# Performance work log

Measured on AMD Instinct MI355X. Metric: run time of the kernel, lower is better.

## Reference

```python
import jax, jax.numpy as jnp
import numpy as np

N_HEAD, N_KV_HEAD, N_EMBD, SEQ_LEN = 16, 4, 1024, 2048
HEAD_DIM = N_EMBD // N_HEAD  # 64
B = 2


def _rope(x, cos, sin):
    # x: [B, T, H, D]; cos/sin: [1, T, 1, D//2]
    d = x.shape[-1] // 2
    x1, x2 = x[..., :d], x[..., d:]
    return jnp.concatenate([x1 * cos + x2 * sin, -x1 * sin + x2 * cos], axis=-1)


def setup_inputs() -> dict:
    key = jax.random.key(0)
    ks = jax.random.split(key, 5)
    x = jax.random.normal(ks[0], (B, SEQ_LEN, N_EMBD), dtype=jnp.float32)
    # real RoPE tables (base 10000)
    half = HEAD_DIM // 2
    inv_freq = 1.0 / (10000.0 ** (jnp.arange(half, dtype=jnp.float32) / half))
    ang = jnp.arange(SEQ_LEN, dtype=jnp.float32)[:, None] * inv_freq[None, :]  # [T, half]
    cos = jnp.cos(ang)[None, :, None, :]  # [1, T, 1, half]
    sin = jnp.sin(ang)[None, :, None, :]
    s = 0.02
    Wq = s * jax.random.normal(ks[1], (N_EMBD, N_HEAD * HEAD_DIM), dtype=jnp.float32)
    Wk = s * jax.random.normal(ks[2], (N_EMBD, N_KV_HEAD * HEAD_DIM), dtype=jnp.float32)
    Wv = s * jax.random.normal(ks[3], (N_EMBD, N_KV_HEAD * HEAD_DIM), dtype=jnp.float32)
    Wo = s * jax.random.normal(ks[4], (N_EMBD, N_EMBD), dtype=jnp.float32)
    return {"x": x, "cos": cos, "sin": sin, "Wq": Wq, "Wk": Wk, "Wv": Wv, "Wo": Wo}


def reference(x, cos, sin, Wq, Wk, Wv, Wo):
    Bsz, T, C = x.shape
    H, Hkv, D = N_HEAD, N_KV_HEAD, HEAD_DIM
    q = (x @ Wq).reshape(Bsz, T, H, D)
    k = (x @ Wk).reshape(Bsz, T, Hkv, D)
    v = (x @ Wv).reshape(Bsz, T, Hkv, D)
    q = _rope(q, cos, sin)
    k = _rope(k, cos, sin)
    # GQA: repeat kv heads to match query heads
    rep = H // Hkv
    k = jnp.repeat(k, rep, axis=2)  # [B, T, H, D]
    v = jnp.repeat(v, rep, axis=2)
    scale = 1.0 / np.sqrt(D).astype(np.float32)
    att = jnp.einsum('bqhd,bkhd->bhqk', q, k) * scale  # [B, H, T, T]
    causal = jnp.tril(jnp.ones((T, T), dtype=bool))
    att = jnp.where(causal[None, None, :, :], att, -jnp.inf)
    att = jax.nn.softmax(att, axis=-1)
    y = jnp.einsum('bhqk,bkhd->bqhd', att, v).reshape(Bsz, T, C)
    return y @ Wo
```

## Files before the change

kernel.cpp:

```cpp
#include <hip/hip_runtime.h>
#include <hip/hip_bf16.h>


typedef __attribute__((ext_vector_type(8))) short s16x8;
typedef __attribute__((ext_vector_type(4))) float f32x4;
typedef __attribute__((ext_vector_type(4))) unsigned short u16x4;

#define LOG2E 1.44269504088896340736f

__device__ __forceinline__ float bf2f(unsigned short u) {
  unsigned int i = ((unsigned int)u) << 16;
  return __builtin_bit_cast(float, i);
}
__device__ __forceinline__ unsigned short f2bf(float f) {
  unsigned int i = __builtin_bit_cast(unsigned int, f);
  i += 0x7fffu + ((i >> 16) & 1u);
  return (unsigned short)(i >> 16);
}

__device__ __forceinline__ void async16(const void* g, void* l) {
  __builtin_amdgcn_global_load_lds(
      (const __attribute__((address_space(1))) void*)g,
      (__attribute__((address_space(3))) void*)l, 16, 0, 0);
}


__global__ void conv_f32_to_bf16(const float* __restrict__ in,
                                 unsigned short* __restrict__ out, int n) {
  int i = (blockIdx.x * blockDim.x + threadIdx.x) * 4;
  if (i + 3 < n) {
    float4 v = *(const float4*)(in + i);
    u16x4 o = { f2bf(v.x), f2bf(v.y), f2bf(v.z), f2bf(v.w) };
    *(u16x4*)(out + i) = o;
  }
}

__global__ void transpose_conv(const float* __restrict__ W,
                               unsigned short* __restrict__ Wt, int K, int N) {
  __shared__ float tile[32][33];
  int n0 = blockIdx.x * 32, k0 = blockIdx.y * 32;
  int tx = threadIdx.x, ty = threadIdx.y;
  for (int i = ty; i < 32; i += 8)
    tile[i][tx] = W[(size_t)(k0 + i) * N + n0 + tx];
  __syncthreads();
  for (int i = ty; i < 32; i += 8)
    Wt[(size_t)(n0 + i) * K + k0 + tx] = f2bf(tile[tx][i]);
}

__global__ void rope_qk(unsigned short* __restrict__ QKV,
                        const float* __restrict__ cosb,
                        const float* __restrict__ sinb) {
  int idx = blockIdx.x * blockDim.x + threadIdx.x;
  int d = idx & 31;
  int hh = (idx >> 5) % 20;
  int row = idx / (32 * 20);
  int t = row & 2047;
  size_t base;
  float mul;
  if (hh < 16) { base = (size_t)row * 1536 + hh * 64 + d;               mul = 0.125f; }
  else         { base = (size_t)row * 1536 + 1024 + (hh - 16) * 64 + d; mul = 1.0f;   }
  float x1 = bf2f(QKV[base]), x2 = bf2f(QKV[base + 32]);
  float c = cosb[t * 32 + d], s = sinb[t * 32 + d];
  QKV[base]      = f2bf((x1 * c + x2 * s) * mul);
  QKV[base + 32] = f2bf((-x1 * s + x2 * c) * mul);
}

__global__ __launch_bounds__(256) void gemm_bt(
    const unsigned short* __restrict__ A, const unsigned short* __restrict__ Bt,
    void* __restrict__ Cp, int M, int N, int K, int c_f32) {
  __shared__ unsigned short As[128 * 64];
  __shared__ unsigned short Bs[64 * 64];
  int tid = threadIdx.x;
  int w = tid >> 6, l = tid & 63, g = l >> 4, lr = l & 15;
  int wr = w >> 1, wc = w & 1;
  int m0 = blockIdx.y * 128, n0 = blockIdx.x * 64;
  int sk = lr & 7;

  f32x4 acc[4][2] = {};

  for (int k0 = 0; k0 < K; k0 += 64) {
#pragma unroll
    for (int i = 0; i < 4; ++i) {
      int c = i * 256 + tid;
      int row = c >> 3, srcu = ((c & 7) ^ (row & 7)) * 8;
      async16(A + (size_t)(m0 + row) * K + k0 + srcu, (char*)As + c * 16);
    }
#pragma unroll
    for (int i = 0; i < 2; ++i) {
      int c = i * 256 + tid;
      int row = c >> 3, srcu = ((c & 7) ^ (row & 7)) * 8;
      async16(Bt + (size_t)(n0 + row) * K + k0 + srcu, (char*)Bs + c * 16);
    }
    __syncthreads();

    s16x8 af[2][4], bfr[2][2];
#pragma unroll
    for (int ks = 0; ks < 2; ++ks) {
#pragma unroll
      for (int m = 0; m < 4; ++m)
        af[ks][m] = *(const s16x8*)(As + (wr * 64 + m * 16 + lr) * 64 +
                                    ((ks * 4 + g) ^ sk) * 8);
#pragma unroll
      for (int n = 0; n < 2; ++n)
        bfr[ks][n] = *(const s16x8*)(Bs + (wc * 32 + n * 16 + lr) * 64 +
                                     ((ks * 4 + g) ^ sk) * 8);
    }
#pragma unroll
    for (int ks = 0; ks < 2; ++ks)
#pragma unroll
      for (int m = 0; m < 4; ++m)
#pragma unroll
        for (int n = 0; n < 2; ++n)
          acc[m][n] = __builtin_amdgcn_mfma_f32_16x16x32_bf16(
              af[ks][m], bfr[ks][n], acc[m][n], 0, 0, 0);
    __syncthreads();
  }

  if (c_f32) {
    float* C = (float*)Cp;
#pragma unroll
    for (int m = 0; m < 4; ++m)
#pragma unroll
      for (int n = 0; n < 2; ++n)
#pragma unroll
        for (int r = 0; r < 4; ++r)
          C[(size_t)(m0 + wr * 64 + m * 16 + g * 4 + r) * N +
            n0 + wc * 32 + n * 16 + lr] = acc[m][n][r];
  } else {
    unsigned short* C = (unsigned short*)Cp;
#pragma unroll
    for (int m = 0; m < 4; ++m)
#pragma unroll
      for (int n = 0; n < 2; ++n)
#pragma unroll
        for (int r = 0; r < 4; ++r)
          C[(size_t)(m0 + wr * 64 + m * 16 + g * 4 + r) * N +
            n0 + wc * 32 + n * 16 + lr] = f2bf(acc[m][n][r]);
  }
}

__global__ __launch_bounds__(256) void attn_fused(
    const unsigned short* __restrict__ QKV, unsigned short* __restrict__ Y) {
  __shared__ unsigned short Kt[2][64 * 64];
  __shared__ unsigned short Vt[2][64 * 64];
  __shared__ unsigned short Pb[4][16 * 64];

  const int T = 2048, CS = 1536;
  int tid = threadIdx.x;
  int w = tid >> 6, l = tid & 63, g = l >> 4, lr = l & 15;
  int n = blockIdx.x;
  int ip = n >> 5;
  int bh = n & 31, b = bh >> 4, h = bh & 15, kvh = h >> 2;
  int sx = lr & 7;

  const unsigned short* Qp = QKV + (size_t)b * T * CS + h * 64;
  const unsigned short* Kp = QKV + (size_t)b * T * CS + 1024 + kvh * 64;
  const unsigned short* Vp = QKV + (size_t)b * T * CS + 1280 + kvh * 64;
  unsigned short* Pw = Pb[w];

  int kvA = tid & 63, dA = (tid >> 6) * 8, dB = dA + 32;

  for (int pass = 0; pass < 2; ++pass) {
    int qt = pass == 0 ? (31 - ip) : ip;
    int qw = qt * 64 + w * 16;
    int q_mine = qw + lr;

    s16x8 qf[2];
#pragma unroll
    for (int ks = 0; ks < 2; ++ks)
      qf[ks] = *(const s16x8*)(Qp + (size_t)q_mine * CS + ks * 32 + g * 8);

    f32x4 o[4] = {};
    float mrun = -1e30f, lrun = 0.f;
    int ntiles = qt + 1;

#pragma unroll
    for (int i = 0; i < 2; ++i) {
      int c = i * 256 + tid;
      int row = c >> 3, srcc = ((c & 7) ^ (row & 7)) * 8;
      async16(Kp + (size_t)row * CS + srcc, (char*)(&Kt[0][0]) + c * 16);
    }
#pragma unroll
    for (int i = 0; i < 2; ++i) {
      int c = i * 256 + tid;
      int kv = c & 63, d0v = (c >> 6) * 8;
      s16x8 vv = *(const s16x8*)(Vp + (size_t)kv * CS + d0v);
#pragma unroll
      for (int j = 0; j < 8; ++j)
        Vt[0][(d0v + j) * 64 + (kv ^ (j * 8))] = (unsigned short)vv[j];
    }
    __syncthreads();

    int cur = 0;
    for (int it = 0; it < ntiles; ++it) {
      int kv0 = it * 64;
      bool hasnext = (it + 1 < ntiles);

      s16x8 vvA, vvB;
      if (hasnext) {
        int kvn = kv0 + 64;
#pragma unroll
        for (int i = 0; i < 2; ++i) {
          int c = i * 256 + tid;
          int row = c >> 3, srcc = ((c & 7) ^ (row & 7)) * 8;
          async16(Kp + (size_t)(kvn + row) * CS + srcc,
                  (char*)(&Kt[cur ^ 1][0]) + c * 16);
        }
        vvA = *(const s16x8*)(Vp + (size_t)(kvn + kvA) * CS + dA);
        vvB = *(const s16x8*)(Vp + (size_t)(kvn + kvA) * CS + dB);
      }

      const unsigned short* Kc = &Kt[cur][0];
      const unsigned short* Vc = &Vt[cur][0];
      f32x4 s[4];
      __builtin_amdgcn_s_setprio(1);
#pragma unroll
      for (int nf = 0; nf < 4; ++nf) {
        f32x4 z = {};
#pragma unroll
        for (int ks = 0; ks < 2; ++ks) {
          s16x8 kf = *(const s16x8*)(Kc + (nf * 16 + lr) * 64 +
                                     ((ks * 4 + g) ^ sx) * 8);
          z = __builtin_amdgcn_mfma_f32_16x16x32_bf16(kf, qf[ks], z, 0, 0, 0);
        }
        s[nf] = z;
      }
      __builtin_amdgcn_s_setprio(0);

      if (it == ntiles - 1) {
#pragma unroll
        for (int nf = 0; nf < 4; ++nf)
#pragma unroll
          for (int r = 0; r < 4; ++r)
            if (kv0 + nf * 16 + g * 4 + r > q_mine) s[nf][r] = -1e30f;
      }

      float mt = s[0][0];
#pragma unroll
      for (int nf = 0; nf < 4; ++nf)
#pragma unroll
        for (int r = 0; r < 4; ++r) mt = fmaxf(mt, s[nf][r]);
      mt = fmaxf(mt, __shfl_xor(mt, 16, 64));
      mt = fmaxf(mt, __shfl_xor(mt, 32, 64));

      if (__any(mt > mrun + 8.f)) {
        float mnew = fmaxf(mrun, mt);
        float corr = exp2f((mrun - mnew) * LOG2E);
        float psum = 0.f;
#pragma unroll
        for (int nf = 0; nf < 4; ++nf)
#pragma unroll
          for (int r = 0; r < 4; ++r) {
            float p = exp2f((s[nf][r] - mnew) * LOG2E);
            s[nf][r] = p;
            psum += p;
          }
        psum += __shfl_xor(psum, 16, 64);
        psum += __shfl_xor(psum, 32, 64);
        lrun = lrun * corr + psum;
        mrun = mnew;
#pragma unroll
        for (int r = 0; r < 4; ++r) {
          float cr = __shfl(corr, g * 4 + r, 64);
#pragma unroll
          for (int d0 = 0; d0 < 4; ++d0) o[d0][r] *= cr;
        }
      } else {
        float psum = 0.f;
#pragma unroll
        for (int nf = 0; nf < 4; ++nf)
#pragma unroll
          for (int r = 0; r < 4; ++r) {
            float p = exp2f((s[nf][r] - mrun) * LOG2E);
            s[nf][r] = p;
            psum += p;
          }
        psum += __shfl_xor(psum, 16, 64);
        psum += __shfl_xor(psum, 32, 64);
        lrun += psum;
      }

#pragma unroll
      for (int nf = 0; nf < 4; ++nf) {
        u16x4 pv = { f2bf(s[nf][0]), f2bf(s[nf][1]),
                     f2bf(s[nf][2]), f2bf(s[nf][3]) };
        *(u16x4*)(Pw + lr * 64 + ((nf * 16 + g * 4) ^ (sx * 8))) = pv;
      }
      asm volatile("s_waitcnt lgkmcnt(0)" ::: "memory");
      __builtin_amdgcn_sched_barrier(0);

      s16x8 pf[2];
#pragma unroll
      for (int ks = 0; ks < 2; ++ks)
        pf[ks] = *(const s16x8*)(Pw + lr * 64 + ((ks * 4 + g) ^ sx) * 8);
      __builtin_amdgcn_s_setprio(1);
#pragma unroll
      for (int d0 = 0; d0 < 4; ++d0)
#pragma unroll
        for (int ks = 0; ks < 2; ++ks) {
          s16x8 vf = *(const s16x8*)(Vc + (d0 * 16 + lr) * 64 +
                                     ((ks * 4 + g) ^ sx) * 8);
          o[d0] = __builtin_amdgcn_mfma_f32_16x16x32_bf16(pf[ks], vf, o[d0], 0, 0, 0);
        }
      __builtin_amdgcn_s_setprio(0);

      if (hasnext) {
#pragma unroll
        for (int j = 0; j < 8; ++j)
          Vt[cur ^ 1][(dA + j) * 64 + (kvA ^ (j * 8))] = (unsigned short)vvA[j];
#pragma unroll
        for (int j = 0; j < 8; ++j)
          Vt[cur ^ 1][(dB + j) * 64 + (kvA ^ (j * 8))] = (unsigned short)vvB[j];
      }
      __syncthreads();
      cur ^= 1;
    }

#pragma unroll
    for (int r = 0; r < 4; ++r) {
      float lv = __shfl(lrun, g * 4 + r, 64);
      float inv = 1.f / lv;
      size_t rowoff = (size_t)(b * T + qw + g * 4 + r) * 1024 + h * 64;
#pragma unroll
      for (int d0 = 0; d0 < 4; ++d0)
        Y[rowoff + d0 * 16 + lr] = f2bf(o[d0][r] * inv);
    }
  }
}


extern "C" void kernel_launch(void* const* d_in, const int* in_sizes, int n_in,
                              void* d_out, int out_size, void* d_ws, size_t ws_size,
                              hipStream_t stream) {
  const float* x    = (const float*)d_in[0];
  const float* cosb = (const float*)d_in[1];
  const float* sinb = (const float*)d_in[2];
  const float* Wq   = (const float*)d_in[3];
  const float* Wk   = (const float*)d_in[4];
  const float* Wv   = (const float*)d_in[5];
  const float* Wo   = (const float*)d_in[6];
  float* out = (float*)d_out;

  char* ob = (char*)d_out;
  char* ws = (char*)d_ws;
  const size_t MB = 1024 * 1024;
  unsigned short* QKVb  = (unsigned short*)(ob);
  unsigned short* xb    = (unsigned short*)(ws);
  unsigned short* Wqkvt = (unsigned short*)(ws + 8 * MB);
  unsigned short* Wot   = (unsigned short*)(ws + 11 * MB);
  unsigned short* Yb    = xb;

  conv_f32_to_bf16<<<4096, 256, 0, stream>>>(x, xb, 4096 * 1024);
  transpose_conv<<<dim3(32, 32), dim3(32, 8), 0, stream>>>(Wq, Wqkvt, 1024, 1024);
  transpose_conv<<<dim3(8, 32), dim3(32, 8), 0, stream>>>(Wk, Wqkvt + (size_t)1024 * 1024, 1024, 256);
  transpose_conv<<<dim3(8, 32), dim3(32, 8), 0, stream>>>(Wv, Wqkvt + (size_t)1280 * 1024, 1024, 256);
  transpose_conv<<<dim3(32, 32), dim3(32, 8), 0, stream>>>(Wo, Wot, 1024, 1024);

  gemm_bt<<<dim3(24, 32), 256, 0, stream>>>(xb, Wqkvt, QKVb, 4096, 1536, 1024, 0);

  rope_qk<<<10240, 256, 0, stream>>>(QKVb, cosb, sinb);

  attn_fused<<<dim3(512), 256, 0, stream>>>(QKVb, Yb);

  gemm_bt<<<dim3(16, 32), 256, 0, stream>>>(Yb, Wot, out, 4096, 1024, 1024, 1);
}
```

Baseline: 132.7 us.

## Split attention KV range across two wave groups and merge partial softmax states

Attention blocks now run 512 threads as two groups of four waves, each handling half of the causal KV tiles for the same query tile, with per-group double-buffered K/V in shared memory. The partial output, max and sum from group 1 are merged into group 0 through shared memory at the end. This shortens the serial KV loop per block so more waves are in flight. It also folds log2(e) into the Q scaling during RoPE to drop a multiply per exp, and uses a packed bf16 convert instruction for P. In exchange it adds an end-of-pass merge, extra barriers, and idle waves when the two halves are uneven.

```diff
diff --git a/kernel.cpp b/kernel.cpp
--- a/kernel.cpp
+++ b/kernel.cpp
@@ -16,6 +16,11 @@
   unsigned int i = __builtin_bit_cast(unsigned int, f);
   i += 0x7fffu + ((i >> 16) & 1u);
   return (unsigned short)(i >> 16);
+}
+__device__ __forceinline__ unsigned int cvtpk(float lo, float hi) {
+  unsigned int r;
+  asm("v_cvt_pk_bf16_f32 %0, %1, %2" : "=v"(r) : "v"(lo), "v"(hi));
+  return r;
 }
 
 __device__ __forceinline__ void async16(const void* g, void* l) {
@@ -57,8 +62,8 @@
   int t = row & 2047;
   size_t base;
   float mul;
-  if (hh < 16) { base = (size_t)row * 1536 + hh * 64 + d;               mul = 0.125f; }
-  else         { base = (size_t)row * 1536 + 1024 + (hh - 16) * 64 + d; mul = 1.0f;   }
+  if (hh < 16) { base = (size_t)row * 1536 + hh * 64 + d;   mul = 0.125f * LOG2E; }
+  else         { base = (size_t)row * 1536 + 1024 + (hh - 16) * 64 + d; mul = 1.0f; }
   float x1 = bf2f(QKV[base]), x2 = bf2f(QKV[base + 32]);
   float c = cosb[t * 32 + d], s = sinb[t * 32 + d];
   QKV[base]      = f2bf((x1 * c + x2 * s) * mul);
@@ -139,30 +144,39 @@
   }
 }
 
-__global__ __launch_bounds__(256) void attn_fused(
+__global__ __launch_bounds__(512, 4) void attn_fused(
     const unsigned short* __restrict__ QKV, unsigned short* __restrict__ Y) {
-  __shared__ unsigned short Kt[2][64 * 64];
-  __shared__ unsigned short Vt[2][64 * 64];
-  __shared__ unsigned short Pb[4][16 * 64];
+  __shared__ char smem[81920];
 
   const int T = 2048, CS = 1536;
   int tid = threadIdx.x;
   int w = tid >> 6, l = tid & 63, g = l >> 4, lr = l & 15;
+  int grp = w >> 2, ws = w & 3, gt = tid & 255;
   int n = blockIdx.x;
   int ip = n >> 5;
   int bh = n & 31, b = bh >> 4, h = bh & 15, kvh = h >> 2;
   int sx = lr & 7;
 
+  unsigned short* Kg = (unsigned short*)(smem + grp * 16384);
+  unsigned short* Vg = (unsigned short*)(smem + 32768 + grp * 16384);
+  unsigned short* Pw = (unsigned short*)(smem + 65536 + w * 2048);
+  float* MO = (float*)(smem);
+  float* MM = (float*)(smem + 16384);
+  float* ML = (float*)(smem + 17408);
+
   const unsigned short* Qp = QKV + (size_t)b * T * CS + h * 64;
   const unsigned short* Kp = QKV + (size_t)b * T * CS + 1024 + kvh * 64;
   const unsigned short* Vp = QKV + (size_t)b * T * CS + 1280 + kvh * 64;
-  unsigned short* Pw = Pb[w];
-
-  int kvA = tid & 63, dA = (tid >> 6) * 8, dB = dA + 32;
+
+  int kvA = gt & 63, dA = (gt >> 6) * 8, dB = dA + 32;
 
   for (int pass = 0; pass < 2; ++pass) {
-    int qt = pass == 0 ? (31 - ip) : ip;
-    int qw = qt * 64 + w * 16;
+    int qt = pass ? ip : (31 - ip);
+    int nt = qt + 1;
+    int H1 = (nt + 1) >> 1;
+    int t0 = grp ? H1 : 0;
+    int cnt = grp ? (nt - H1) : H1;
+    int qw = qt * 64 + ws * 16;
     int q_mine = qw + lr;
 
     s16x8 qf[2];
@@ -172,158 +186,189 @@
 
     f32x4 o[4] = {};
     float mrun = -1e30f, lrun = 0.f;
-    int ntiles = qt + 1;
-
-#pragma unroll
-    for (int i = 0; i < 2; ++i) {
-      int c = i * 256 + tid;
-      int row = c >> 3, srcc = ((c & 7) ^ (row & 7)) * 8;
-      async16(Kp + (size_t)row * CS + srcc, (char*)(&Kt[0][0]) + c * 16);
-    }
-#pragma unroll
-    for (int i = 0; i < 2; ++i) {
-      int c = i * 256 + tid;
-      int kv = c & 63, d0v = (c >> 6) * 8;
-      s16x8 vv = *(const s16x8*)(Vp + (size_t)kv * CS + d0v);
-#pragma unroll
-      for (int j = 0; j < 8; ++j)
-        Vt[0][(d0v + j) * 64 + (kv ^ (j * 8))] = (unsigned short)vv[j];
-    }
+
     __syncthreads();
 
+    if (cnt > 0) {
+#pragma unroll
+      for (int i = 0; i < 2; ++i) {
+        int c = i * 256 + gt;
+        int row = c >> 3, srcc = ((c & 7) ^ (row & 7)) * 8;
+        async16(Kp + (size_t)(t0 * 64 + row) * CS + srcc, (char*)Kg + c * 16);
+      }
+#pragma unroll
+      for (int i = 0; i < 2; ++i) {
+        int c = i * 256 + gt;
+        int kv = c & 63, d0v = (c >> 6) * 8;
+        s16x8 vv = *(const s16x8*)(Vp + (size_t)(t0 * 64 + kv) * CS + d0v);
+#pragma unroll
+        for (int j = 0; j < 8; ++j)
+          Vg[(d0v + j) * 64 + (kv ^ (j * 8))] = (unsigned short)vv[j];
+      }
+    }
+    __syncthreads();
+
     int cur = 0;
-    for (int it = 0; it < ntiles; ++it) {
-      int kv0 = it * 64;
-      bool hasnext = (it + 1 < ntiles);
+    for (int j = 0; j < H1; ++j) {
+      int tj = t0 + j;
+      bool active = (j < cnt);
+      bool hasnext = (j + 1 < cnt);
+      int kv0 = tj * 64;
 
       s16x8 vvA, vvB;
       if (hasnext) {
         int kvn = kv0 + 64;
 #pragma unroll
         for (int i = 0; i < 2; ++i) {
-          int c = i * 256 + tid;
+          int c = i * 256 + gt;
           int row = c >> 3, srcc = ((c & 7) ^ (row & 7)) * 8;
           async16(Kp + (size_t)(kvn + row) * CS + srcc,
-                  (char*)(&Kt[cur ^ 1][0]) + c * 16);
+                  (char*)Kg + (cur ^ 1) * 8192 + c * 16);
         }
         vvA = *(const s16x8*)(Vp + (size_t)(kvn + kvA) * CS + dA);
         vvB = *(const s16x8*)(Vp + (size_t)(kvn + kvA) * CS + dB);
       }
 
-      const unsigned short* Kc = &Kt[cur][0];
-      const unsigned short* Vc = &Vt[cur][0];
-      f32x4 s[4];
-      __builtin_amdgcn_s_setprio(1);
-#pragma unroll
-      for (int nf = 0; nf < 4; ++nf) {
-        f32x4 z = {};
-#pragma unroll
-        for (int ks = 0; ks < 2; ++ks) {
-          s16x8 kf = *(const s16x8*)(Kc + (nf * 16 + lr) * 64 +
-                                     ((ks * 4 + g) ^ sx) * 8);
-          z = __builtin_amdgcn_mfma_f32_16x16x32_bf16(kf, qf[ks], z, 0, 0, 0);
-        }
-        s[nf] = z;
-      }
-      __builtin_amdgcn_s_setprio(0);
-
-      if (it == ntiles - 1) {
+      if (active) {
+        const unsigned short* Kc = Kg + cur * 4096;
+        const unsigned short* Vc = Vg + cur * 4096;
+        f32x4 s[4];
+        __builtin_amdgcn_s_setprio(1);
+#pragma unroll
+        for (int nf = 0; nf < 4; ++nf) {
+          f32x4 z = {};
+#pragma unroll
+          for (int ks = 0; ks < 2; ++ks) {
+            s16x8 kf = *(const s16x8*)(Kc + (nf * 16 + lr) * 64 +
+                                       ((ks * 4 + g) ^ sx) * 8);
+            z = __builtin_amdgcn_mfma_f32_16x16x32_bf16(kf, qf[ks], z, 0, 0, 0);
+          }
+          s[nf] = z;
+        }
+        __builtin_amdgcn_s_setprio(0);
+
+        if (tj == nt - 1) {
+#pragma unroll
+          for (int nf = 0; nf < 4; ++nf)
+#pragma unroll
+            for (int r = 0; r < 4; ++r)
+              if (kv0 + nf * 16 + g * 4 + r > q_mine) s[nf][r] = -1e30f;
+        }
+
+        float mt = s[0][0];
 #pragma unroll
         for (int nf = 0; nf < 4; ++nf)
 #pragma unroll
-          for (int r = 0; r < 4; ++r)
-            if (kv0 + nf * 16 + g * 4 + r > q_mine) s[nf][r] = -1e30f;
-      }
-
-      float mt = s[0][0];
-#pragma unroll
-      for (int nf = 0; nf < 4; ++nf)
-#pragma unroll
-        for (int r = 0; r < 4; ++r) mt = fmaxf(mt, s[nf][r]);
-      mt = fmaxf(mt, __shfl_xor(mt, 16, 64));
-      mt = fmaxf(mt, __shfl_xor(mt, 32, 64));
-
-      if (__any(mt > mrun + 8.f)) {
-        float mnew = fmaxf(mrun, mt);
-        float corr = exp2f((mrun - mnew) * LOG2E);
-        float psum = 0.f;
-#pragma unroll
-        for (int nf = 0; nf < 4; ++nf)
+          for (int r = 0; r < 4; ++r) mt = fmaxf(mt, s[nf][r]);
+        mt = fmaxf(mt, __shfl_xor(mt, 16, 64));
+        mt = fmaxf(mt, __shfl_xor(mt, 32, 64));
+
+        if (__any(mt > mrun + 11.5416f)) {
+          float mnew = fmaxf(mrun, mt);
+          float corr = exp2f(mrun - mnew);
+          float psum = 0.f;
+#pragma unroll
+          for (int nf = 0; nf < 4; ++nf)
+#pragma unroll
+            for (int r = 0; r < 4; ++r) {
+              float p = exp2f(s[nf][r] - mnew);
+              s[nf][r] = p;
+              psum += p;
+            }
+          psum += __shfl_xor(psum, 16, 64);
+          psum += __shfl_xor(psum, 32, 64);
+          lrun = lrun * corr + psum;
+          mrun = mnew;
 #pragma unroll
           for (int r = 0; r < 4; ++r) {
-            float p = exp2f((s[nf][r] - mnew) * LOG2E);
-            s[nf][r] = p;
-            psum += p;
+            float cr = __shfl(corr, g * 4 + r, 64);
+#pragma unroll
+            for (int d0 = 0; d0 < 4; ++d0) o[d0][r] *= cr;
           }
-        psum += __shfl_xor(psum, 16, 64);
-        psum += __shfl_xor(psum, 32, 64);
-        lrun = lrun * corr + psum;
-        mrun = mnew;
-#pragma unroll
-        for (int r = 0; r < 4; ++r) {
-          float cr = __shfl(corr, g * 4 + r, 64);
-#pragma unroll
-          for (int d0 = 0; d0 < 4; ++d0) o[d0][r] *= cr;
-        }
-      } else {
-        float psum = 0.f;
-#pragma unroll
-        for (int nf = 0; nf < 4; ++nf)
-#pragma unroll
-          for (int r = 0; r < 4; ++r) {
-            float p = exp2f((s[nf][r] - mrun) * LOG2E);
-            s[nf][r] = p;
-            psum += p;
+        } else {
+          float psum = 0.f;
+#pragma unroll
+          for (int nf = 0; nf < 4; ++nf)
+#pragma unroll
+            for (int r = 0; r < 4; ++r) {
+              float p = exp2f(s[nf][r] - mrun);
+              s[nf][r] = p;
+              psum += p;
+            }
+          psum += __shfl_xor(psum, 16, 64);
+          psum += __shfl_xor(psum, 32, 64);
+          lrun += psum;
+        }
+
+#pragma unroll
+        for (int nf = 0; nf < 4; ++nf) {
+          uint2 pv;
+          pv.x = cvtpk(s[nf][0], s[nf][1]);
+          pv.y = cvtpk(s[nf][2], s[nf][3]);
+          *(uint2*)(Pw + lr * 64 + ((nf * 16 + g * 4) ^ (sx * 8))) = pv;
+        }
+        asm volatile("s_waitcnt lgkmcnt(0)" ::: "memory");
+        __builtin_amdgcn_sched_barrier(0);
+
+        s16x8 pf[2];
+#pragma unroll
+        for (int ks = 0; ks < 2; ++ks)
+          pf[ks] = *(const s16x8*)(Pw + lr * 64 + ((ks * 4 + g) ^ sx) * 8);
+        __builtin_amdgcn_s_setprio(1);
+#pragma unroll
+        for (int d0 = 0; d0 < 4; ++d0)
+#pragma unroll
+          for (int ks = 0; ks < 2; ++ks) {
+            s16x8 vf = *(const s16x8*)(Vc + (d0 * 16 + lr) * 64 +
+                                       ((ks * 4 + g) ^ sx) * 8);
+            o[d0] = __builtin_amdgcn_mfma_f32_16x16x32_bf16(pf[ks], vf, o[d0], 0, 0, 0);
           }
-        psum += __shfl_xor(psum, 16, 64);
-        psum += __shfl_xor(psum, 32, 64);
-        lrun += psum;
-      }
-
-#pragma unroll
-      for (int nf = 0; nf < 4; ++nf) {
-        u16x4 pv = { f2bf(s[nf][0]), f2bf(s[nf][1]),
-                     f2bf(s[nf][2]), f2bf(s[nf][3]) };
-        *(u16x4*)(Pw + lr * 64 + ((nf * 16 + g * 4) ^ (sx * 8))) = pv;
-      }
-      asm volatile("s_waitcnt lgkmcnt(0)" ::: "memory");
-      __builtin_amdgcn_sched_barrier(0);
-
-      s16x8 pf[2];
-#pragma unroll
-      for (int ks = 0; ks < 2; ++ks)
-        pf[ks] = *(const s16x8*)(Pw + lr * 64 + ((ks * 4 + g) ^ sx) * 8);
-      __builtin_amdgcn_s_setprio(1);
-#pragma unroll
-      for (int d0 = 0; d0 < 4; ++d0)
-#pragma unroll
-        for (int ks = 0; ks < 2; ++ks) {
-          s16x8 vf = *(const s16x8*)(Vc + (d0 * 16 + lr) * 64 +
-                                     ((ks * 4 + g) ^ sx) * 8);
-          o[d0] = __builtin_amdgcn_mfma_f32_16x16x32_bf16(pf[ks], vf, o[d0], 0, 0, 0);
-        }
-      __builtin_amdgcn_s_setprio(0);
+        __builtin_amdgcn_s_setprio(0);
+      }
 
       if (hasnext) {
 #pragma unroll
-        for (int j = 0; j < 8; ++j)
-          Vt[cur ^ 1][(dA + j) * 64 + (kvA ^ (j * 8))] = (unsigned short)vvA[j];
-#pragma unroll
-        for (int j = 0; j < 8; ++j)
-          Vt[cur ^ 1][(dB + j) * 64 + (kvA ^ (j * 8))] = (unsigned short)vvB[j];
+        for (int j2 = 0; j2 < 8; ++j2)
+          Vg[cur == 0 ? 4096 + (dA + j2) * 64 + (kvA ^ (j2 * 8))
+                      : (dA + j2) * 64 + (kvA ^ (j2 * 8))] = (unsigned short)vvA[j2];
+#pragma unroll
+        for (int j2 = 0; j2 < 8; ++j2)
+          Vg[cur == 0 ? 4096 + (dB + j2) * 64 + (kvA ^ (j2 * 8))
+                      : (dB + j2) * 64 + (kvA ^ (j2 * 8))] = (unsigned short)vvB[j2];
       }
       __syncthreads();
       cur ^= 1;
     }
 
-#pragma unroll
-    for (int r = 0; r < 4; ++r) {
-      float lv = __shfl(lrun, g * 4 + r, 64);
-      float inv = 1.f / lv;
-      size_t rowoff = (size_t)(b * T + qw + g * 4 + r) * 1024 + h * 64;
+    int mbase = ws * 64 + l;
+    if (grp == 1) {
 #pragma unroll
       for (int d0 = 0; d0 < 4; ++d0)
-        Y[rowoff + d0 * 16 + lr] = f2bf(o[d0][r] * inv);
+#pragma unroll
+        for (int r = 0; r < 4; ++r)
+          MO[(d0 * 4 + r) * 256 + mbase] = o[d0][r];
+      MM[mbase] = mrun;
+      ML[mbase] = lrun;
+    }
+    __syncthreads();
+    if (grp == 0) {
+      float m1 = MM[mbase], l1 = ML[mbase];
+      float mS = fmaxf(mrun, m1);
+      float c0 = exp2f(mrun - mS), c1 = exp2f(m1 - mS);
+      float lS = lrun * c0 + l1 * c1;
+#pragma unroll
+      for (int r = 0; r < 4; ++r) {
+        float cr0 = __shfl(c0, g * 4 + r, 64);
+        float cr1 = __shfl(c1, g * 4 + r, 64);
+        float lv  = __shfl(lS, g * 4 + r, 64);
+        float inv = 1.f / lv;
+        size_t rowoff = (size_t)(b * T + qw + g * 4 + r) * 1024 + h * 64;
+#pragma unroll
+        for (int d0 = 0; d0 < 4; ++d0) {
+          float om = o[d0][r] * cr0 + MO[(d0 * 4 + r) * 256 + mbase] * cr1;
+          Y[rowoff + d0 * 16 + lr] = f2bf(om * inv);
+        }
+      }
     }
   }
 }
@@ -360,7 +405,7 @@
 
   rope_qk<<<10240, 256, 0, stream>>>(QKVb, cosb, sinb);
 
-  attn_fused<<<dim3(512), 256, 0, stream>>>(QKVb, Yb);
+  attn_fused<<<dim3(512), 512, 0, stream>>>(QKVb, Yb);
 
   gemm_bt<<<dim3(16, 32), 256, 0, stream>>>(Yb, Wot, out, 4096, 1024, 1024, 1);
 }
```

New measurement: 177.7 us. +34.0%, slower.

## Rewrite attention with 32x32 MFMA, register-resident P, and one q-tile per block

Applied to the files above, without the earlier changes.

The attention kernel moves from 16x16x32 to 32x32x16 bf16 MFMA with two waves of 32 query rows each. The P matrix now stays in registers, packed with v_cvt_pk_bf16 and exchanged across half-waves by shuffle, so the LDS round trip and waitcnt are gone. The log2(e) factor is folded into the Q scaling during RoPE so the softmax can call exp2 directly. The grid changes from 512 blocks that each did a paired long and short q-tile to 1024 blocks of 128 threads with one q-tile each, which drops the manual causal load balancing and leaves it to the scheduler.

```diff
diff --git a/kernel.cpp b/kernel.cpp
--- a/kernel.cpp
+++ b/kernel.cpp
@@ -3,8 +3,10 @@
 
 
 typedef __attribute__((ext_vector_type(8))) short s16x8;
+typedef __attribute__((ext_vector_type(16))) float f32x16;
 typedef __attribute__((ext_vector_type(4))) float f32x4;
 typedef __attribute__((ext_vector_type(4))) unsigned short u16x4;
+typedef __attribute__((ext_vector_type(4))) unsigned int u32x4;
 
 #define LOG2E 1.44269504088896340736f
 
@@ -16,6 +18,11 @@
   unsigned int i = __builtin_bit_cast(unsigned int, f);
   i += 0x7fffu + ((i >> 16) & 1u);
   return (unsigned short)(i >> 16);
+}
+__device__ __forceinline__ unsigned int cvtpk(float lo, float hi) {
+  unsigned int r;
+  asm("v_cvt_pk_bf16_f32 %0, %1, %2" : "=v"(r) : "v"(lo), "v"(hi));
+  return r;
 }
 
 __device__ __forceinline__ void async16(const void* g, void* l) {
@@ -57,8 +64,8 @@
   int t = row & 2047;
   size_t base;
   float mul;
-  if (hh < 16) { base = (size_t)row * 1536 + hh * 64 + d;               mul = 0.125f; }
-  else         { base = (size_t)row * 1536 + 1024 + (hh - 16) * 64 + d; mul = 1.0f;   }
+  if (hh < 16) { base = (size_t)row * 1536 + hh * 64 + d;   mul = 0.125f * LOG2E; }
+  else         { base = (size_t)row * 1536 + 1024 + (hh - 16) * 64 + d; mul = 1.0f; }
   float x1 = bf2f(QKV[base]), x2 = bf2f(QKV[base + 32]);
   float c = cosb[t * 32 + d], s = sinb[t * 32 + d];
   QKV[base]      = f2bf((x1 * c + x2 * s) * mul);
@@ -139,192 +146,182 @@
   }
 }
 
-__global__ __launch_bounds__(256) void attn_fused(
+__global__ __launch_bounds__(128) void attn_fused(
     const unsigned short* __restrict__ QKV, unsigned short* __restrict__ Y) {
   __shared__ unsigned short Kt[2][64 * 64];
   __shared__ unsigned short Vt[2][64 * 64];
-  __shared__ unsigned short Pb[4][16 * 64];
 
   const int T = 2048, CS = 1536;
   int tid = threadIdx.x;
-  int w = tid >> 6, l = tid & 63, g = l >> 4, lr = l & 15;
+  int wv = tid >> 6, l = tid & 63;
+  int lq = l & 31, hi = l >> 5;
   int n = blockIdx.x;
-  int ip = n >> 5;
+  int qt = 31 - (n >> 5);
   int bh = n & 31, b = bh >> 4, h = bh & 15, kvh = h >> 2;
-  int sx = lr & 7;
+  int sx = l & 7;
+  int qw = qt * 64 + wv * 32;
+  int q_mine = qw + lq;
 
   const unsigned short* Qp = QKV + (size_t)b * T * CS + h * 64;
   const unsigned short* Kp = QKV + (size_t)b * T * CS + 1024 + kvh * 64;
   const unsigned short* Vp = QKV + (size_t)b * T * CS + 1280 + kvh * 64;
-  unsigned short* Pw = Pb[w];
-
-  int kvA = tid & 63, dA = (tid >> 6) * 8, dB = dA + 32;
-
-  for (int pass = 0; pass < 2; ++pass) {
-    int qt = pass == 0 ? (31 - ip) : ip;
-    int qw = qt * 64 + w * 16;
-    int q_mine = qw + lr;
-
-    s16x8 qf[2];
-#pragma unroll
-    for (int ks = 0; ks < 2; ++ks)
-      qf[ks] = *(const s16x8*)(Qp + (size_t)q_mine * CS + ks * 32 + g * 8);
-
-    f32x4 o[4] = {};
-    float mrun = -1e30f, lrun = 0.f;
-    int ntiles = qt + 1;
-
-#pragma unroll
-    for (int i = 0; i < 2; ++i) {
-      int c = i * 256 + tid;
-      int row = c >> 3, srcc = ((c & 7) ^ (row & 7)) * 8;
-      async16(Kp + (size_t)row * CS + srcc, (char*)(&Kt[0][0]) + c * 16);
-    }
-#pragma unroll
-    for (int i = 0; i < 2; ++i) {
-      int c = i * 256 + tid;
-      int kv = c & 63, d0v = (c >> 6) * 8;
-      s16x8 vv = *(const s16x8*)(Vp + (size_t)kv * CS + d0v);
-#pragma unroll
-      for (int j = 0; j < 8; ++j)
-        Vt[0][(d0v + j) * 64 + (kv ^ (j * 8))] = (unsigned short)vv[j];
+
+  s16x8 qf[4];
+#pragma unroll
+  for (int ks = 0; ks < 4; ++ks)
+    qf[ks] = *(const s16x8*)(Qp + (size_t)q_mine * CS + ks * 16 + hi * 8);
+
+  f32x16 o0 = {}, o1 = {};
+  float mrun = -1e30f, lrun = 0.f;
+
+  int ntiles = qt + 1;
+  int kvi = (tid & 15) * 4, dc = (tid >> 4) * 8;
+
+#pragma unroll
+  for (int i = 0; i < 4; ++i) {
+    int c = i * 128 + tid;
+    int row = c >> 3, srcu = ((c & 7) ^ (row & 7)) * 8;
+    async16(Kp + (size_t)row * CS + srcu, (char*)(&Kt[0][0]) + c * 16);
+  }
+  {
+    s16x8 v0 = *(const s16x8*)(Vp + (size_t)(kvi + 0) * CS + dc);
+    s16x8 v1 = *(const s16x8*)(Vp + (size_t)(kvi + 1) * CS + dc);
+    s16x8 v2 = *(const s16x8*)(Vp + (size_t)(kvi + 2) * CS + dc);
+    s16x8 v3 = *(const s16x8*)(Vp + (size_t)(kvi + 3) * CS + dc);
+#pragma unroll
+    for (int j = 0; j < 8; ++j) {
+      u16x4 pk = { (unsigned short)v0[j], (unsigned short)v1[j],
+                   (unsigned short)v2[j], (unsigned short)v3[j] };
+      *(u16x4*)(&Vt[0][0] + (dc + j) * 64 + (kvi ^ (j * 8))) = pk;
+    }
+  }
+  __syncthreads();
+
+  int cur = 0;
+  for (int it = 0; it < ntiles; ++it) {
+    int kv0 = it * 64;
+    bool hasnext = (it + 1 < ntiles);
+
+    s16x8 v0, v1, v2, v3;
+    if (hasnext) {
+      int kvn = kv0 + 64;
+#pragma unroll
+      for (int i = 0; i < 4; ++i) {
+        int c = i * 128 + tid;
+        int row = c >> 3, srcu = ((c & 7) ^ (row & 7)) * 8;
+        async16(Kp + (size_t)(kvn + row) * CS + srcu,
+                (char*)(&Kt[cur ^ 1][0]) + c * 16);
+      }
+      v0 = *(const s16x8*)(Vp + (size_t)(kvn + kvi + 0) * CS + dc);
+      v1 = *(const s16x8*)(Vp + (size_t)(kvn + kvi + 1) * CS + dc);
+      v2 = *(const s16x8*)(Vp + (size_t)(kvn + kvi + 2) * CS + dc);
+      v3 = *(const s16x8*)(Vp + (size_t)(kvn + kvi + 3) * CS + dc);
+    }
+
+    const unsigned short* Kc = &Kt[cur][0];
+    const unsigned short* Vc = &Vt[cur][0];
+
+    f32x16 s0 = {}, s1 = {};
+    __builtin_amdgcn_s_setprio(1);
+#pragma unroll
+    for (int ks = 0; ks < 4; ++ks) {
+      int u = ((ks * 2 + hi) ^ sx) * 8;
+      s16x8 kf0 = *(const s16x8*)(Kc + lq * 64 + u);
+      s16x8 kf1 = *(const s16x8*)(Kc + (32 + lq) * 64 + u);
+      s0 = __builtin_amdgcn_mfma_f32_32x32x16_bf16(kf0, qf[ks], s0, 0, 0, 0);
+      s1 = __builtin_amdgcn_mfma_f32_32x32x16_bf16(kf1, qf[ks], s1, 0, 0, 0);
+    }
+    __builtin_amdgcn_s_setprio(0);
+
+    if (it == ntiles - 1) {
+#pragma unroll
+      for (int r = 0; r < 16; ++r) {
+        int kvg = kv0 + (r & 3) + 8 * (r >> 2) + 4 * hi;
+        if (kvg > q_mine) s0[r] = -1e30f;
+        if (kvg + 32 > q_mine) s1[r] = -1e30f;
+      }
+    }
+
+    float mt = s0[0];
+#pragma unroll
+    for (int r = 1; r < 16; ++r) mt = fmaxf(mt, s0[r]);
+#pragma unroll
+    for (int r = 0; r < 16; ++r) mt = fmaxf(mt, s1[r]);
+    mt = fmaxf(mt, __shfl_xor(mt, 32, 64));
+
+    if (__any(mt > mrun + 11.5416f)) {
+      float mnew = fmaxf(mrun, mt);
+      float corr = exp2f(mrun - mnew);
+      float psum = 0.f;
+#pragma unroll
+      for (int r = 0; r < 16; ++r) {
+        float p0 = exp2f(s0[r] - mnew); s0[r] = p0; psum += p0;
+        float p1 = exp2f(s1[r] - mnew); s1[r] = p1; psum += p1;
+      }
+      psum += __shfl_xor(psum, 32, 64);
+      lrun = lrun * corr + psum;
+      mrun = mnew;
+#pragma unroll
+      for (int r = 0; r < 16; ++r) { o0[r] *= corr; o1[r] *= corr; }
+    } else {
+      float psum = 0.f;
+#pragma unroll
+      for (int r = 0; r < 16; ++r) {
+        float p0 = exp2f(s0[r] - mrun); s0[r] = p0; psum += p0;
+        float p1 = exp2f(s1[r] - mrun); s1[r] = p1; psum += p1;
+      }
+      psum += __shfl_xor(psum, 32, 64);
+      lrun += psum;
+    }
+
+    __builtin_amdgcn_s_setprio(1);
+#pragma unroll
+    for (int ks = 0; ks < 4; ++ks) {
+      int rb = (ks & 1) * 8;
+      const f32x16& sp = (ks < 2) ? s0 : s1;
+      unsigned int X0 = cvtpk(sp[rb + 0], sp[rb + 1]);
+      unsigned int X1 = cvtpk(sp[rb + 2], sp[rb + 3]);
+      unsigned int Y0 = cvtpk(sp[rb + 4], sp[rb + 5]);
+      unsigned int Y1 = cvtpk(sp[rb + 6], sp[rb + 7]);
+      unsigned int Z0 = hi ? X0 : Y0;
+      unsigned int Z1 = hi ? X1 : Y1;
+      unsigned int Zp0 = (unsigned int)__shfl_xor((int)Z0, 32, 64);
+      unsigned int Zp1 = (unsigned int)__shfl_xor((int)Z1, 32, 64);
+      u32x4 pw = { hi ? Zp0 : X0, hi ? Zp1 : X1,
+                   hi ? Y0 : Zp0, hi ? Y1 : Zp1 };
+      s16x8 pf = __builtin_bit_cast(s16x8, pw);
+      int u = ((ks * 2 + hi) ^ sx) * 8;
+      s16x8 vf0 = *(const s16x8*)(Vc + lq * 64 + u);
+      s16x8 vf1 = *(const s16x8*)(Vc + (32 + lq) * 64 + u);
+      o0 = __builtin_amdgcn_mfma_f32_32x32x16_bf16(vf0, pf, o0, 0, 0, 0);
+      o1 = __builtin_amdgcn_mfma_f32_32x32x16_bf16(vf1, pf, o1, 0, 0, 0);
+    }
+    __builtin_amdgcn_s_setprio(0);
+
+    if (hasnext) {
+      unsigned short* Vn = &Vt[cur ^ 1][0];
+#pragma unroll
+      for (int j = 0; j < 8; ++j) {
+        u16x4 pk = { (unsigned short)v0[j], (unsigned short)v1[j],
+                     (unsigned short)v2[j], (unsigned short)v3[j] };
+        *(u16x4*)(Vn + (dc + j) * 64 + (kvi ^ (j * 8))) = pk;
+      }
     }
     __syncthreads();
-
-    int cur = 0;
-    for (int it = 0; it < ntiles; ++it) {
-      int kv0 = it * 64;
-      bool hasnext = (it + 1 < ntiles);
-
-      s16x8 vvA, vvB;
-      if (hasnext) {
-        int kvn = kv0 + 64;
-#pragma unroll
-        for (int i = 0; i < 2; ++i) {
-          int c = i * 256 + tid;
-          int row = c >> 3, srcc = ((c & 7) ^ (row & 7)) * 8;
-          async16(Kp + (size_t)(kvn + row) * CS + srcc,
-                  (char*)(&Kt[cur ^ 1][0]) + c * 16);
-        }
-        vvA = *(const s16x8*)(Vp + (size_t)(kvn + kvA) * CS + dA);
-        vvB = *(const s16x8*)(Vp + (size_t)(kvn + kvA) * CS + dB);
-      }
-
-      const unsigned short* Kc = &Kt[cur][0];
-      const unsigned short* Vc = &Vt[cur][0];
-      f32x4 s[4];
-      __builtin_amdgcn_s_setprio(1);
-#pragma unroll
-      for (int nf = 0; nf < 4; ++nf) {
-        f32x4 z = {};
-#pragma unroll
-        for (int ks = 0; ks < 2; ++ks) {
-          s16x8 kf = *(const s16x8*)(Kc + (nf * 16 + lr) * 64 +
-                                     ((ks * 4 + g) ^ sx) * 8);
-          z = __builtin_amdgcn_mfma_f32_16x16x32_bf16(kf, qf[ks], z, 0, 0, 0);
-        }
-        s[nf] = z;
-      }
-      __builtin_amdgcn_s_setprio(0);
-
-      if (it == ntiles - 1) {
-#pragma unroll
-        for (int nf = 0; nf < 4; ++nf)
-#pragma unroll
-          for (int r = 0; r < 4; ++r)
-            if (kv0 + nf * 16 + g * 4 + r > q_mine) s[nf][r] = -1e30f;
-      }
-
-      float mt = s[0][0];
-#pragma unroll
-      for (int nf = 0; nf < 4; ++nf)
-#pragma unroll
-        for (int r = 0; r < 4; ++r) mt = fmaxf(mt, s[nf][r]);
-      mt = fmaxf(mt, __shfl_xor(mt, 16, 64));
-      mt = fmaxf(mt, __shfl_xor(mt, 32, 64));
-
-      if (__any(mt > mrun + 8.f)) {
-        float mnew = fmaxf(mrun, mt);
-        float corr = exp2f((mrun - mnew) * LOG2E);
-        float psum = 0.f;
-#pragma unroll
-        for (int nf = 0; nf < 4; ++nf)
-#pragma unroll
-          for (int r = 0; r < 4; ++r) {
-            float p = exp2f((s[nf][r] - mnew) * LOG2E);
-            s[nf][r] = p;
-            psum += p;
-          }
-        psum += __shfl_xor(psum, 16, 64);
-        psum += __shfl_xor(psum, 32, 64);
-        lrun = lrun * corr + psum;
-        mrun = mnew;
-#pragma unroll
-        for (int r = 0; r < 4; ++r) {
-          float cr = __shfl(corr, g * 4 + r, 64);
-#pragma unroll
-          for (int d0 = 0; d0 < 4; ++d0) o[d0][r] *= cr;
-        }
-      } else {
-        float psum = 0.f;
-#pragma unroll
-        for (int nf = 0; nf < 4; ++nf)
-#pragma unroll
-          for (int r = 0; r < 4; ++r) {
-            float p = exp2f((s[nf][r] - mrun) * LOG2E);
-            s[nf][r] = p;
-            psum += p;
-          }
-        psum += __shfl_xor(psum, 16, 64);
-        psum += __shfl_xor(psum, 32, 64);
-        lrun += psum;
-      }
-
-#pragma unroll
-      for (int nf = 0; nf < 4; ++nf) {
-        u16x4 pv = { f2bf(s[nf][0]), f2bf(s[nf][1]),
-                     f2bf(s[nf][2]), f2bf(s[nf][3]) };
-        *(u16x4*)(Pw + lr * 64 + ((nf * 16 + g * 4) ^ (sx * 8))) = pv;
-      }
-      asm volatile("s_waitcnt lgkmcnt(0)" ::: "memory");
-      __builtin_amdgcn_sched_barrier(0);
-
-      s16x8 pf[2];
-#pragma unroll
-      for (int ks = 0; ks < 2; ++ks)
-        pf[ks] = *(const s16x8*)(Pw + lr * 64 + ((ks * 4 + g) ^ sx) * 8);
-      __builtin_amdgcn_s_setprio(1);
-#pragma unroll
-      for (int d0 = 0; d0 < 4; ++d0)
-#pragma unroll
-        for (int ks = 0; ks < 2; ++ks) {
-          s16x8 vf = *(const s16x8*)(Vc + (d0 * 16 + lr) * 64 +
-                                     ((ks * 4 + g) ^ sx) * 8);
-          o[d0] = __builtin_amdgcn_mfma_f32_16x16x32_bf16(pf[ks], vf, o[d0], 0, 0, 0);
-        }
-      __builtin_amdgcn_s_setprio(0);
-
-      if (hasnext) {
-#pragma unroll
-        for (int j = 0; j < 8; ++j)
-          Vt[cur ^ 1][(dA + j) * 64 + (kvA ^ (j * 8))] = (unsigned short)vvA[j];
-#pragma unroll
-        for (int j = 0; j < 8; ++j)
-          Vt[cur ^ 1][(dB + j) * 64 + (kvA ^ (j * 8))] = (unsigned short)vvB[j];
-      }
-      __syncthreads();
-      cur ^= 1;
-    }
-
-#pragma unroll
-    for (int r = 0; r < 4; ++r) {
-      float lv = __shfl(lrun, g * 4 + r, 64);
-      float inv = 1.f / lv;
-      size_t rowoff = (size_t)(b * T + qw + g * 4 + r) * 1024 + h * 64;
-#pragma unroll
-      for (int d0 = 0; d0 < 4; ++d0)
-        Y[rowoff + d0 * 16 + lr] = f2bf(o[d0][r] * inv);
-    }
+    cur ^= 1;
+  }
+
+  float inv = 1.f / lrun;
+  size_t rowoff = (size_t)(b * T + q_mine) * 1024 + h * 64;
+#pragma unroll
+  for (int rr = 0; rr < 4; ++rr) {
+    int d0 = rr * 8 + 4 * hi;
+    u16x4 w0 = { f2bf(o0[rr * 4 + 0] * inv), f2bf(o0[rr * 4 + 1] * inv),
+                 f2bf(o0[rr * 4 + 2] * inv), f2bf(o0[rr * 4 + 3] * inv) };
+    *(u16x4*)(Y + rowoff + d0) = w0;
+    u16x4 w1 = { f2bf(o1[rr * 4 + 0] * inv), f2bf(o1[rr * 4 + 1] * inv),
+                 f2bf(o1[rr * 4 + 2] * inv), f2bf(o1[rr * 4 + 3] * inv) };
+    *(u16x4*)(Y + rowoff + 32 + d0) = w1;
   }
 }
 
@@ -360,7 +357,7 @@
 
   rope_qk<<<10240, 256, 0, stream>>>(QKVb, cosb, sinb);
 
-  attn_fused<<<dim3(512), 256, 0, stream>>>(QKVb, Yb);
+  attn_fused<<<dim3(1024), 128, 0, stream>>>(QKVb, Yb);
 
   gemm_bt<<<dim3(16, 32), 256, 0, stream>>>(Yb, Wot, out, 4096, 1024, 1024, 1);
 }
```

Result: slower. 142.9 us (+7.7%).
